# Kernel optimization log

Measured on AMD Instinct MI355X. Metric: run time of the kernel, lower is better.

Reference implementation:

```python
import jax, jax.numpy as jnp
import numpy as np

# Static hyperparameters (match init_kwargs)
PAD = 4          # one_side_pad_length
KL = 9           # kernel_size (= 2*PAD + 1 so L_out == output_size with stride 1)
STRIDE = 1
NLC = 8          # num_sparse_LC
OUT = 4096       # output_size


def _repeat_lengths():
    padded = OUT + 2 * PAD                      # 4104
    rough = padded // NLC                       # 513
    lens = []
    total = 0
    for i in range(NLC):
        if i == NLC - 1:
            cover = OUT - total
        else:
            cover = rough - 2 * PAD
        lens.append(cover)
        total += cover
    return lens                                  # [505]*7 + [561]


def setup_inputs() -> dict:
    key = jax.random.key(0)
    k1, k2, k3 = jax.random.split(key, 3)
    x = jax.random.normal(k1, (8, 2, 4, 64, 4096), dtype=jnp.float32)
    # weight: (dim_d, dim_k, out, in, num_sparse_LC, 1, kernel_size)
    weight = jax.random.normal(k2, (2, 4, 64, 64, 8, 1, 9), dtype=jnp.float32) * 0.05
    # conv_bias_param: (dim_d, dim_k, out, num_sparse_LC, 1)
    conv_bias_param = jax.random.normal(k3, (2, 4, 64, 8, 1), dtype=jnp.float32) * 0.02
    return {"x": x, "weight": weight, "conv_bias_param": conv_bias_param}


def reference(x, weight, conv_bias_param):
    # x: (b, d, k, in, L)
    x_pad = jnp.pad(x, ((0, 0), (0, 0), (0, 0), (0, 0), (PAD, PAD)))
    # unfold(-1, KL, 1): x_unf[..., l, f] = x_pad[..., l + f]; shape (b,d,k,in,OUT,KL)
    x_unf = jnp.stack([x_pad[..., f:f + OUT] for f in range(KL)], axis=-1)
    lens = _repeat_lengths()
    outs = []
    start = 0
    for i in range(NLC):  # small fixed loop over segments (avoids repeated-weight materialization)
        ln = lens[i]
        w = weight[:, :, :, :, i, 0, :]                 # (d, k, o, in, kl)
        xs = x_unf[:, :, :, :, start:start + ln, :]     # (b, d, k, in, ln, kl)
        o = jnp.einsum('dkoif,bdkilf->bdkol', w, xs)    # (b, d, k, o, ln)
        o = o + conv_bias_param[None, :, :, :, i, :]    # bias broadcasts over b and l
        outs.append(o)
        start += ln
    return jnp.concatenate(outs, axis=-1)               # (b, d, k, o, OUT)
```

## Files before the change

kernel.cpp:

```cpp
#include <hip/hip_runtime.h>

typedef __attribute__((ext_vector_type(8))) short bf16x8;
typedef __attribute__((ext_vector_type(4))) float f32x4;

#define WT2_BYTES (8ull * 8 * 9 * 8192)

static __device__ __forceinline__ ushort f2bf(float f) {
    union { float f; unsigned u; } v; v.f = f;
    unsigned r = v.u + 0x7FFF + ((v.u >> 16) & 1);
    return (ushort)(r >> 16);
}
static __device__ __forceinline__ unsigned cvtpk(float a, float b) {
    unsigned r;
    asm("v_cvt_pk_bf16_f32 %0, %1, %2" : "=v"(r) : "v"(a), "v"(b));
    return r;
}

__global__ __launch_bounds__(256) void wprep3_kernel(const float* __restrict__ w,
                                                     ushort* __restrict__ wt) {
    __shared__ float raw[4608];
    __shared__ ushort row[72 * 64];
    int bid = blockIdx.x;
    int dk = bid >> 6, o = bid & 63;
    const float* src = w + (size_t)bid * 4608;
    int t = threadIdx.x;
    #pragma unroll
    for (int j = 0; j < 18; ++j) raw[t + 256 * j] = src[t + 256 * j];
    __syncthreads();
    int osw = o & 7;
    #pragma unroll
    for (int p = 0; p < 18; ++p) {
        int idx = t + 256 * p;
        int cf = idx >> 6, i = idx & 63;
        int c = cf / 9, f = cf - c * 9;
        row[cf * 64 + ((i >> 3) ^ osw) * 8 + (i & 7)] = f2bf(raw[i * 72 + c * 9 + f]);
    }
    __syncthreads();
    char* wb = (char*)wt + (size_t)dk * 8 * 9 * 8192 + o * 128;
    #pragma unroll
    for (int q = 0; q < 3; ++q) {
        int idx = q * 256 + t;
        if (idx < 576) {
            int cf = idx >> 3, cc = idx & 7;
            *(uint4*)(wb + (size_t)cf * 8192 + cc * 16) = *(const uint4*)&row[cf * 64 + cc * 8];
        }
    }
}

__global__ __launch_bounds__(256, 2) void conv5_kernel(
    const float* __restrict__ x, const ushort* __restrict__ wt,
    const float* __restrict__ bias, float* __restrict__ out)
{
    __shared__ __align__(16) ushort XL[264 * 64];

    int bid = blockIdx.x;
    int b = bid / 136, rem = bid - b * 136;
    int dk = rem / 17, tile = rem - dk * 17;
    int c, lt;
    if (tile < 14) { c = tile >> 1; lt = tile & 1; } else { c = 7; lt = tile - 14; }
    int Sc = 505 * c, lb = lt << 8;
    int V = ((c == 7) ? 561 : 505) - lb; if (V > 256) V = 256;
    int bdk = b * 8 + dk;
    int R0 = Sc + lb;

    int t = threadIdx.x, lane = t & 63, wv = t >> 6;
    int ln16 = lane & 15, g = lane >> 4, Lw = wv << 6;

    const char* wsl = (const char*)wt + (size_t)(dk * 8 + c) * 9 * 8192 + ln16 * 128;
    const char* wlA = wsl + ((g ^ (ln16 & 7)) * 16);
    const char* wlB = wsl + (((4 + g) ^ (ln16 & 7)) * 16);

    bf16x8 w0[2][4], w1[2][4];
    auto loadW = [&](bf16x8 (&dst)[2][4], int f) {
        const char* bA = wlA + f * 8192;
        const char* bB = wlB + f * 8192;
        #pragma unroll
        for (int q = 0; q < 4; ++q) {
            dst[0][q] = *(const bf16x8*)(bA + q * 2048);
            dst[1][q] = *(const bf16x8*)(bB + q * 2048);
        }
    };

    loadW(w0, 0);

    {
        const float* xb = x + ((size_t)(bdk * 64 + wv * 16)) * 4096;
        bool edge = (R0 < 4) || (R0 > 3836);
        #pragma unroll
        for (int k = 0; k < 5; ++k) {
            int r = k * 64 + lane;
            if (r < 264) {
                int xr = R0 + r - 4;
                float v[16];
                if (!edge) {
                    #pragma unroll
                    for (int j = 0; j < 16; ++j) v[j] = xb[(size_t)j * 4096 + xr];
                } else {
                    bool ok = (xr >= 0) && (xr < 4096);
                    int xc = ok ? xr : 0;
                    #pragma unroll
                    for (int j = 0; j < 16; ++j) v[j] = ok ? xb[(size_t)j * 4096 + xc] : 0.0f;
                }
                uint4 A, B;
                A.x = cvtpk(v[0], v[1]);   A.y = cvtpk(v[2], v[3]);
                A.z = cvtpk(v[4], v[5]);   A.w = cvtpk(v[6], v[7]);
                B.x = cvtpk(v[8], v[9]);   B.y = cvtpk(v[10], v[11]);
                B.z = cvtpk(v[12], v[13]); B.w = cvtpk(v[14], v[15]);
                char* base = (char*)XL + r * 128;
                *(uint4*)(base + (((2 * wv)     ^ (r & 7)) * 16)) = A;
                *(uint4*)(base + (((2 * wv + 1) ^ (r & 7)) * 16)) = B;
            }
        }
    }
    loadW(w1, 1);
    __syncthreads();

    f32x4 acc[4][4];
    #pragma unroll
    for (int a0 = 0; a0 < 4; ++a0)
        #pragma unroll
        for (int a1 = 0; a1 < 4; ++a1) acc[a0][a1] = (f32x4){0.f, 0.f, 0.f, 0.f};

    auto tap = [&](bf16x8 (&wf)[2][4], int f) {
        int rbase = Lw + ln16 + f;
        int swz = rbase & 7;
        #pragma unroll
        for (int s = 0; s < 2; ++s) {
            int cof = ((s * 4 + g) ^ swz) * 16;
            bf16x8 av[4];
            #pragma unroll
            for (int mf = 0; mf < 4; ++mf)
                av[mf] = *(const bf16x8*)((const char*)XL + (rbase + mf * 16) * 128 + cof);
            #pragma unroll
            for (int mf = 0; mf < 4; ++mf)
                #pragma unroll
                for (int nf = 0; nf < 4; ++nf)
                    acc[mf][nf] = __builtin_amdgcn_mfma_f32_16x16x32_bf16(av[mf], wf[s][nf], acc[mf][nf], 0, 0, 0);
        }
    };

    tap(w0, 0); loadW(w0, 2);
    tap(w1, 1); loadW(w1, 3);
    tap(w0, 2); loadW(w0, 4);
    tap(w1, 3); loadW(w1, 5);
    tap(w0, 4); loadW(w0, 6);
    tap(w1, 5); loadW(w1, 7);
    tap(w0, 6); loadW(w0, 8);
    tap(w1, 7);
    tap(w0, 8);

    float* ob = out + ((size_t)(bdk * 64)) * 4096 + Sc + lb;
    #pragma unroll
    for (int nf = 0; nf < 4; ++nf) {
        int o = nf * 16 + ln16;
        float bvs = bias[(dk * 64 + o) * 8 + c];
        #pragma unroll
        for (int mf = 0; mf < 4; ++mf) {
            int l = Lw + mf * 16 + g * 4;
            f32x4 vv = acc[mf][nf];
            vv[0] += bvs; vv[1] += bvs; vv[2] += bvs; vv[3] += bvs;
            if (l + 4 <= V) {
                *(f32x4*)(ob + (size_t)o * 4096 + l) = vv;
            } else if (l < V) {
                #pragma unroll
                for (int r = 0; r < 4; ++r)
                    if (l + r < V) ob[(size_t)o * 4096 + l + r] = vv[r];
            }
        }
    }
}

extern "C" void kernel_launch(void* const* d_in, const int* in_sizes, int n_in,
                              void* d_out, int out_size, void* d_ws, size_t ws_size,
                              hipStream_t stream) {
    const float* x    = (const float*)d_in[0];
    const float* wgt  = (const float*)d_in[1];
    const float* bias = (const float*)d_in[2];
    float* out        = (float*)d_out;
    ushort* wt2       = (ushort*)d_ws;

    hipLaunchKernelGGL(wprep3_kernel, dim3(512), dim3(256), 0, stream, wgt, wt2);
    hipLaunchKernelGGL(conv5_kernel, dim3(1088), dim3(256), 0, stream, x, wt2, bias, out);
}
```

Baseline: 52.05 us.

## Halve conv tiles, split waves 2x2, stage weights in LDS via async loads

Each block now covers 128 output positions instead of 256, giving 2112 blocks, and its four waves form a 2x2 grid over positions and output channels. Weight taps are no longer held in registers. They are double-buffered in shared memory using global_load_lds and read back per MFMA step, with a barrier after each tap. Launch bounds go from 2 to 4 blocks per CU to improve occupancy and latency hiding, at the cost of a larger relative x-halo overhead, more total weight traffic and per-tap synchronisation.

Result: slower. 56.13 us (+7.8%).

```diff
diff --git a/kernel.cpp b/kernel.cpp
--- a/kernel.cpp
+++ b/kernel.cpp
@@ -4,6 +4,9 @@
 typedef __attribute__((ext_vector_type(4))) float f32x4;
 
 #define WT2_BYTES (8ull * 8 * 9 * 8192)
+
+#define AS1C(p) ((const __attribute__((address_space(1))) void*)(p))
+#define AS3(p)  ((__attribute__((address_space(3))) void*)(p))
 
 static __device__ __forceinline__ ushort f2bf(float f) {
     union { float f; unsigned u; } v; v.f = f;
@@ -47,49 +50,43 @@
     }
 }
 
-__global__ __launch_bounds__(256, 2) void conv5_kernel(
+__global__ __launch_bounds__(256, 4) void conv6_kernel(
     const float* __restrict__ x, const ushort* __restrict__ wt,
     const float* __restrict__ bias, float* __restrict__ out)
 {
-    __shared__ __align__(16) ushort XL[264 * 64];
+    __shared__ __align__(16) ushort XL[136 * 64];
+    __shared__ __align__(16) ushort WL[2 * 4096];
 
     int bid = blockIdx.x;
-    int b = bid / 136, rem = bid - b * 136;
-    int dk = rem / 17, tile = rem - dk * 17;
+    int bdk = bid / 33, tile = bid - bdk * 33;
+    int dk = bdk & 7;
     int c, lt;
-    if (tile < 14) { c = tile >> 1; lt = tile & 1; } else { c = 7; lt = tile - 14; }
-    int Sc = 505 * c, lb = lt << 8;
-    int V = ((c == 7) ? 561 : 505) - lb; if (V > 256) V = 256;
-    int bdk = b * 8 + dk;
+    if (tile < 28) { c = tile >> 2; lt = tile & 3; } else { c = 7; lt = tile - 28; }
+    int Sc = 505 * c, lb = lt << 7;
+    int V = ((c == 7) ? 561 : 505) - lb; if (V > 128) V = 128;
     int R0 = Sc + lb;
 
     int t = threadIdx.x, lane = t & 63, wv = t >> 6;
-    int ln16 = lane & 15, g = lane >> 4, Lw = wv << 6;
+    int ln16 = lane & 15, g = lane >> 4;
+    int wr = wv >> 1, wc = wv & 1;
+    int Lw = wr << 6, Ow = wc << 5;
 
-    const char* wsl = (const char*)wt + (size_t)(dk * 8 + c) * 9 * 8192 + ln16 * 128;
-    const char* wlA = wsl + ((g ^ (ln16 & 7)) * 16);
-    const char* wlB = wsl + (((4 + g) ^ (ln16 & 7)) * 16);
-
-    bf16x8 w0[2][4], w1[2][4];
-    auto loadW = [&](bf16x8 (&dst)[2][4], int f) {
-        const char* bA = wlA + f * 8192;
-        const char* bB = wlB + f * 8192;
-        #pragma unroll
-        for (int q = 0; q < 4; ++q) {
-            dst[0][q] = *(const bf16x8*)(bA + q * 2048);
-            dst[1][q] = *(const bf16x8*)(bB + q * 2048);
-        }
+    const char* wsl = (const char*)wt + (size_t)(dk * 8 + c) * 9 * 8192;
+    auto stageW = [&](int f, int buf) {
+        __builtin_amdgcn_global_load_lds(AS1C(wsl + (size_t)f * 8192 + t * 16),
+                                         AS3((char*)WL + buf * 8192 + t * 16), 16, 0, 0);
+        __builtin_amdgcn_global_load_lds(AS1C(wsl + (size_t)f * 8192 + 4096 + t * 16),
+                                         AS3((char*)WL + buf * 8192 + 4096 + t * 16), 16, 0, 0);
     };
-
-    loadW(w0, 0);
+    stageW(0, 0);
 
     {
         const float* xb = x + ((size_t)(bdk * 64 + wv * 16)) * 4096;
-        bool edge = (R0 < 4) || (R0 > 3836);
+        bool edge = (R0 < 4) || (R0 > 3964);
         #pragma unroll
-        for (int k = 0; k < 5; ++k) {
+        for (int k = 0; k < 3; ++k) {
             int r = k * 64 + lane;
-            if (r < 264) {
+            if (r < 136) {
                 int xr = R0 + r - 4;
                 float v[16];
                 if (!edge) {
@@ -112,47 +109,44 @@
             }
         }
     }
-    loadW(w1, 1);
     __syncthreads();
 
-    f32x4 acc[4][4];
+    f32x4 acc[4][2];
     #pragma unroll
     for (int a0 = 0; a0 < 4; ++a0)
         #pragma unroll
-        for (int a1 = 0; a1 < 4; ++a1) acc[a0][a1] = (f32x4){0.f, 0.f, 0.f, 0.f};
+        for (int a1 = 0; a1 < 2; ++a1) acc[a0][a1] = (f32x4){0.f, 0.f, 0.f, 0.f};
 
-    auto tap = [&](bf16x8 (&wf)[2][4], int f) {
+    #pragma unroll 1
+    for (int f = 0; f < 9; ++f) {
+        int buf = f & 1;
+        if (f < 8) stageW(f + 1, buf ^ 1);
         int rbase = Lw + ln16 + f;
         int swz = rbase & 7;
         #pragma unroll
         for (int s = 0; s < 2; ++s) {
             int cof = ((s * 4 + g) ^ swz) * 16;
-            bf16x8 av[4];
+            int wof = buf * 8192 + ((s * 4 + g) ^ (ln16 & 7)) * 16;
+            bf16x8 av[4], bv[2];
             #pragma unroll
             for (int mf = 0; mf < 4; ++mf)
                 av[mf] = *(const bf16x8*)((const char*)XL + (rbase + mf * 16) * 128 + cof);
             #pragma unroll
+            for (int nf = 0; nf < 2; ++nf)
+                bv[nf] = *(const bf16x8*)((const char*)WL + wof + (Ow + nf * 16 + ln16) * 128);
+            #pragma unroll
             for (int mf = 0; mf < 4; ++mf)
                 #pragma unroll
-                for (int nf = 0; nf < 4; ++nf)
-                    acc[mf][nf] = __builtin_amdgcn_mfma_f32_16x16x32_bf16(av[mf], wf[s][nf], acc[mf][nf], 0, 0, 0);
+                for (int nf = 0; nf < 2; ++nf)
+                    acc[mf][nf] = __builtin_amdgcn_mfma_f32_16x16x32_bf16(av[mf], bv[nf], acc[mf][nf], 0, 0, 0);
         }
-    };
-
-    tap(w0, 0); loadW(w0, 2);
-    tap(w1, 1); loadW(w1, 3);
-    tap(w0, 2); loadW(w0, 4);
-    tap(w1, 3); loadW(w1, 5);
-    tap(w0, 4); loadW(w0, 6);
-    tap(w1, 5); loadW(w1, 7);
-    tap(w0, 6); loadW(w0, 8);
-    tap(w1, 7);
-    tap(w0, 8);
+        if (f < 8) __syncthreads();
+    }
 
     float* ob = out + ((size_t)(bdk * 64)) * 4096 + Sc + lb;
     #pragma unroll
-    for (int nf = 0; nf < 4; ++nf) {
-        int o = nf * 16 + ln16;
+    for (int nf = 0; nf < 2; ++nf) {
+        int o = Ow + nf * 16 + ln16;
         float bvs = bias[(dk * 64 + o) * 8 + c];
         #pragma unroll
         for (int mf = 0; mf < 4; ++mf) {
@@ -180,5 +174,5 @@
     ushort* wt2       = (ushort*)d_ws;
 
     hipLaunchKernelGGL(wprep3_kernel, dim3(512), dim3(256), 0, stream, wgt, wt2);
-    hipLaunchKernelGGL(conv5_kernel, dim3(1088), dim3(256), 0, stream, x, wt2, bias, out);
+    hipLaunchKernelGGL(conv6_kernel, dim3(2112), dim3(256), 0, stream, x, wt2, bias, out);
 }
```
